# Performance work log

Hardware: AMD Instinct MI355X
Metric: run time of the kernel (lower is better)

## Reference

```python
import jax, jax.numpy as jnp
import numpy as np

CAPS = 16          # num_capsules
DIM = 16           # capsule_dim
NUM_ROUTING = 3
L2_EPS = 1e-12     # tf.nn.l2_normalize epsilon


def setup_inputs() -> dict:
    key = jax.random.key(0)
    k1, k2 = jax.random.split(key)
    inputs = jax.random.normal(k1, (16, 64, 64, 128), dtype=jnp.float32)
    # Conv2D kernel, HWIO layout, fan-in scaled like glorot-ish init
    kernel = jax.random.normal(k2, (3, 3, 128, CAPS * DIM), dtype=jnp.float32) * 0.03
    bias = jnp.zeros((CAPS * DIM,), dtype=jnp.float32)
    return {"inputs": inputs, "kernel": kernel, "bias": bias}


def reference(inputs, kernel, bias):
    # Conv2D(caps*dim, 3x3, padding='same', activation='relu'), channels_last
    x = jax.lax.conv_general_dilated(
        inputs, kernel, window_strides=(1, 1), padding="SAME",
        dimension_numbers=("NHWC", "HWIO", "NHWC"))
    x = jax.nn.relu(x + bias)
    B, H, W, _ = x.shape
    x = x.reshape(B, H * W, CAPS, DIM)            # (B, N, C, D)
    b = jnp.zeros((B, H * W, CAPS), dtype=x.dtype)
    v = None
    for _ in range(NUM_ROUTING):
        c = jax.nn.softmax(b, axis=-1)             # over capsules
        s = jnp.einsum("bnc,bncd->bcd", c, x)      # weighted sum over spatial
        # tf.nn.l2_normalize along last axis
        v = s * jax.lax.rsqrt(jnp.maximum(jnp.sum(s * s, axis=-1, keepdims=True), L2_EPS))
        b = b + jnp.einsum("bncd,bcd->bnc", x, v)  # agreement update
    # tile v over spatial dims: (B,1,1,C*D) -> (B,H,W,C*D)
    out = jnp.broadcast_to(v.reshape(B, 1, 1, CAPS * DIM), (B, H, W, CAPS * DIM))
    return out
```

## Files before the change

kernel.cpp:

```cpp
#include <hip/hip_runtime.h>
#include <hip/hip_bf16.h>

typedef unsigned short u16;
typedef unsigned int   u32;

typedef __bf16 bf16x8 __attribute__((ext_vector_type(8)));
typedef float  f32x4  __attribute__((ext_vector_type(4)));

#define GLDS(gp, lp) __builtin_amdgcn_global_load_lds( \
    (const __attribute__((address_space(1))) void*)(gp), \
    (__attribute__((address_space(3))) void*)(lp), 16, 0, 0)

__device__ __forceinline__ u16 f2b(float f) {
    __hip_bfloat16 h = __float2bfloat16(f);
    u16 u; __builtin_memcpy(&u, &h, 2); return u;
}
__device__ __forceinline__ float blo(u32 u) { return __uint_as_float(u << 16); }
__device__ __forceinline__ float bhi(u32 u) { return __uint_as_float(u & 0xffff0000u); }

__global__ void k_prep(const float* __restrict__ in, const float* __restrict__ wk,
                       u16* __restrict__ pad, u16* __restrict__ BF,
                       float* __restrict__ stats) {
    int bx = blockIdx.x, tid = threadIdx.x;
    if (bx < 4356) {
        int idx = bx * 256 + tid;
        int e0  = idx * 8;
        int ch  = e0 & 127;
        int rest = e0 >> 7;
        int pw = rest % 66;
        int r2 = rest / 66;
        int ph = r2 % 66;
        int b  = r2 / 66;
        u16 ov[8];
        if (ph >= 1 && ph <= 64 && pw >= 1 && pw <= 64) {
            const float* src = in + (((b * 64 + (ph - 1)) * 64 + (pw - 1)) * 128 + ch);
            const float4* s4 = (const float4*)src;
            float4 f0 = s4[0], f1 = s4[1];
            ov[0]=f2b(f0.x); ov[1]=f2b(f0.y); ov[2]=f2b(f0.z); ov[3]=f2b(f0.w);
            ov[4]=f2b(f1.x); ov[5]=f2b(f1.y); ov[6]=f2b(f1.z); ov[7]=f2b(f1.w);
        } else {
            #pragma unroll
            for (int j = 0; j < 8; ++j) ov[j] = 0;
        }
        uint4 w; __builtin_memcpy(&w, ov, 16);
        *(uint4*)(pad + e0) = w;
    } else if (bx < 5508) {
        int t = (bx - 4356) * 256 + tid;
        int j  = t & 7;
        int n  = (t >> 3) & 255;
        int q  = (t >> 11) & 3;
        int kk = (t >> 13) & 3;
        int p  = t >> 15;
        BF[t] = f2b(wk[(p * 128 + kk * 32 + q * 8 + j) * 256 + n]);
    } else {
        stats[(bx - 5508) * 256 + tid] = 0.f;
    }
}

__launch_bounds__(256, 2)
__global__ void k_conv(const u16* __restrict__ Ap, const u16* __restrict__ BF,
                       const float* __restrict__ bias,
                       u16* __restrict__ X, float* __restrict__ s0) {
    __shared__ u16 ldsA[12672];
    const int t = threadIdx.x;
    const int lane = t & 63, wid = t >> 6;
    const int q = lane >> 4, l15 = lane & 15;
    const int bb = blockIdx.x >> 6;
    const int h  = blockIdx.x & 63;
    const int wn0 = wid << 6;

#define STAGE(S) { \
    const int sb0 = wid * 396; \
    _Pragma("unroll") for (int i = 0; i < 6; ++i) { \
        int sb = sb0 + i * 64; \
        int slot = sb + lane; \
        int pr = slot / 528; int rem = slot - pr * 528; \
        int wp = rem >> 3, cs = rem & 7; \
        int gc = (S) * 8 + (cs ^ (wp & 7)); \
        const u16* g = Ap + ((((bb * 66 + h + pr) * 66 + wp) << 7) + (gc << 3)); \
        GLDS(g, (char*)ldsA + sb * 16); \
    } \
    { int sb = sb0 + 384; \
      if (lane < 12) { \
        int slot = sb + lane; \
        int pr = slot / 528; int rem = slot - pr * 528; \
        int wp = rem >> 3, cs = rem & 7; \
        int gc = (S) * 8 + (cs ^ (wp & 7)); \
        const u16* g = Ap + ((((bb * 66 + h + pr) * 66 + wp) << 7) + (gc << 3)); \
        GLDS(g, (char*)ldsA + sb * 16); \
      } } }

#define LOADB(B, P, S) { \
    _Pragma("unroll") for (int kk = 0; kk < 2; ++kk) \
    _Pragma("unroll") for (int ni = 0; ni < 4; ++ni) \
        B[kk * 4 + ni] = *(const bf16x8*)(BFl + (P) * 32768 + \
                                          ((S) * 2 + kk) * 8192 + ni * 128); }

#define COMPP(B, DH, DW) { \
    _Pragma("unroll") for (int kk = 0; kk < 2; ++kk) { \
        bf16x8 af[4]; \
        _Pragma("unroll") for (int mi = 0; mi < 4; ++mi) { \
            int wp = mi * 16 + l15 + (DW); \
            int swz = (kk * 4 + q) ^ (wp & 7); \
            af[mi] = *(const bf16x8*)((const char*)ldsA + \
                (((DH) * 528 + wp * 8 + swz) << 4)); \
        } \
        _Pragma("unroll") for (int mi = 0; mi < 4; ++mi) \
        _Pragma("unroll") for (int ni = 0; ni < 4; ++ni) \
            acc[mi][ni] = __builtin_amdgcn_mfma_f32_16x16x32_bf16( \
                af[mi], B[kk * 4 + ni], acc[mi][ni], 0, 0, 0); } }

    const u16* BFl = BF + (q * 2048 + (wn0 + l15) * 8);

    f32x4 zero = {0.f, 0.f, 0.f, 0.f};
    f32x4 acc[4][4];
    #pragma unroll
    for (int mi = 0; mi < 4; ++mi)
        #pragma unroll
        for (int ni = 0; ni < 4; ++ni) acc[mi][ni] = zero;

    bf16x8 B0[8], B1[8];

    STAGE(0);
    __syncthreads();
    LOADB(B0, 0, 0);
    LOADB(B1, 1, 0); COMPP(B0, 0, 0);
    LOADB(B0, 2, 0); COMPP(B1, 0, 1);
    LOADB(B1, 3, 0); COMPP(B0, 0, 2);
    LOADB(B0, 4, 0); COMPP(B1, 1, 0);
    LOADB(B1, 5, 0); COMPP(B0, 1, 1);
    LOADB(B0, 6, 0); COMPP(B1, 1, 2);
    LOADB(B1, 7, 0); COMPP(B0, 2, 0);
    LOADB(B0, 8, 0); COMPP(B1, 2, 1);
    COMPP(B0, 2, 2);
    __syncthreads();

    STAGE(1);
    __syncthreads();
    LOADB(B0, 0, 1);
    LOADB(B1, 1, 1); COMPP(B0, 0, 0);
    LOADB(B0, 2, 1); COMPP(B1, 0, 1);
    LOADB(B1, 3, 1); COMPP(B0, 0, 2);
    LOADB(B0, 4, 1); COMPP(B1, 1, 0);
    LOADB(B1, 5, 1); COMPP(B0, 1, 1);
    LOADB(B0, 6, 1); COMPP(B1, 1, 2);
    LOADB(B1, 7, 1); COMPP(B0, 2, 0);
    LOADB(B0, 8, 1); COMPP(B1, 2, 1);
    COMPP(B0, 2, 2);

    float bv[4];
    #pragma unroll
    for (int ni = 0; ni < 4; ++ni) bv[ni] = bias[wn0 + ni * 16 + l15];
    float colsum[4] = {0.f, 0.f, 0.f, 0.f};
    u16* xrow = X + (((bb << 12) + (h << 6) + q * 4) * 256) + wn0 + l15;
    #pragma unroll
    for (int mi = 0; mi < 4; ++mi) {
        #pragma unroll
        for (int rr = 0; rr < 4; ++rr) {
            u16* xp = xrow + (mi * 16 + rr) * 256;
            #pragma unroll
            for (int ni = 0; ni < 4; ++ni) {
                float v = acc[mi][ni][rr] + bv[ni];
                v = v > 0.f ? v : 0.f;
                xp[ni * 16] = f2b(v);
                colsum[ni] += v;
            }
        }
    }
    #pragma unroll
    for (int ni = 0; ni < 4; ++ni) {
        float c = colsum[ni];
        c += __shfl_xor(c, 16);
        c += __shfl_xor(c, 32);
        if (lane < 16) atomicAdd(&s0[bb * 256 + wn0 + ni * 16 + l15], c);
    }
#undef STAGE
#undef LOADB
#undef COMPP
}

__launch_bounds__(256, 4)
__global__ void k_pass(const u16* __restrict__ X, const float* __restrict__ Sa,
                       const float* __restrict__ Sb, float* __restrict__ Sout,
                       int use2) {
    __shared__ float v1s[272], v2s[272];
    __shared__ float red[4 * 272];
    const int t = threadIdx.x, b = blockIdx.y, chunk = blockIdx.x;
    const int c = t & 15, nl = t >> 4;
    const int lane = t & 63, wid = t >> 6;
    {
        float sa = Sa[b * 256 + t];
        float ss = sa * sa;
        #pragma unroll
        for (int off = 1; off < 16; off <<= 1) ss += __shfl_xor(ss, off);
        ss = ss < 1e-12f ? 1e-12f : ss;
        v1s[(t >> 4) * 17 + (t & 15)] = sa / sqrtf(ss);
        if (use2) {
            float sb = Sb[b * 256 + t];
            float s2v = sb * sb;
            #pragma unroll
            for (int off = 1; off < 16; off <<= 1) s2v += __shfl_xor(s2v, off);
            s2v = s2v < 1e-12f ? 1e-12f : s2v;
            v2s[(t >> 4) * 17 + (t & 15)] = sb / sqrtf(s2v);
        } else {
            v2s[(t >> 4) * 17 + (t & 15)] = 0.f;
        }
    }
    const u16* xbase = X + ((b << 12) + chunk * 64 + nl) * 256 + c * 16;
    uint4 pa[8];
    #pragma unroll
    for (int r = 0; r < 4; ++r) {
        pa[2 * r]     = ((const uint4*)(xbase + r * 16 * 256))[0];
        pa[2 * r + 1] = ((const uint4*)(xbase + r * 16 * 256))[1];
    }
    __syncthreads();
    float v1r[16], v2r[16];
    #pragma unroll
    for (int d = 0; d < 16; ++d) { v1r[d] = v1s[c * 17 + d]; v2r[d] = v2s[c * 17 + d]; }

    float acc[16];
    #pragma unroll
    for (int d = 0; d < 16; ++d) acc[d] = 0.f;

    #pragma unroll
    for (int r = 0; r < 4; ++r) {
        u32 us[8];
        __builtin_memcpy(us, &pa[2 * r], 32);
        float xf[16];
        #pragma unroll
        for (int j = 0; j < 8; ++j) { xf[2*j] = blo(us[j]); xf[2*j+1] = bhi(us[j]); }
        float d1 = 0.f, d2 = 0.f;
        #pragma unroll
        for (int d = 0; d < 16; ++d) {
            d1 += xf[d] * v1r[d];
            d2 += xf[d] * v2r[d];
        }
        float bvv = use2 ? (d1 + d2) : d1;
        float e = __expf(bvv);
        float sm = e;
        #pragma unroll
        for (int off = 1; off < 16; off <<= 1) sm += __shfl_xor(sm, off);
        float w = e / sm;
        #pragma unroll
        for (int d = 0; d < 16; ++d) acc[d] += w * xf[d];
    }
    #pragma unroll
    for (int d = 0; d < 16; ++d) {
        acc[d] += __shfl_xor(acc[d], 16);
        acc[d] += __shfl_xor(acc[d], 32);
    }
    if (lane < 16) {
        #pragma unroll
        for (int d = 0; d < 16; ++d) red[wid * 272 + lane * 17 + d] = acc[d];
    }
    __syncthreads();
    {
        int c2 = t >> 4, d2 = t & 15;
        float tot = red[c2 * 17 + d2]       + red[272 + c2 * 17 + d2]
                  + red[544 + c2 * 17 + d2] + red[816 + c2 * 17 + d2];
        atomicAdd(&Sout[b * 256 + t], tot);
    }
}

__launch_bounds__(256, 4)
__global__ void k_bcast(const float* __restrict__ S, float* __restrict__ Out) {
    __shared__ float vls[256];
    int t = threadIdx.x, bx = blockIdx.x, b = blockIdx.y;
    float s = S[b * 256 + t];
    float ss = s * s;
    #pragma unroll
    for (int off = 1; off < 16; off <<= 1) ss += __shfl_xor(ss, off);
    ss = ss < 1e-12f ? 1e-12f : ss;
    vls[t] = s / sqrtf(ss);
    __syncthreads();
    float4 myv = ((const float4*)vls)[t & 63];
    float4* o = (float4*)Out + (long)b * 262144 + bx * 4096;
    #pragma unroll
    for (int j = 0; j < 16; ++j) o[j * 256 + t] = myv;
}

extern "C" void kernel_launch(void* const* d_in, const int* in_sizes, int n_in,
                              void* d_out, int out_size, void* d_ws, size_t ws_size,
                              hipStream_t stream) {
    const float* in   = (const float*)d_in[0];
    const float* wk   = (const float*)d_in[1];
    const float* bias = (const float*)d_in[2];
    float* out = (float*)d_out;
    char* ws = (char*)d_ws;

    const size_t OFF_PAD = 0;
    const size_t OFF_BF  = 17842176;
    const size_t OFF_X   = 18432000;
    const size_t OFF_ST  = 51986432;
    const size_t NEEDED  = OFF_ST + 3 * 16384;
    if (ws_size < NEEDED) return;

    u16* pad = (u16*)(ws + OFF_PAD);
    u16* BF  = (u16*)(ws + OFF_BF);
    u16* X   = (u16*)(ws + OFF_X);
    float* s0 = (float*)(ws + OFF_ST);
    float* s2 = s0 + 4096;
    float* s3 = s2 + 4096;

    k_prep <<<5556, 256, 0, stream>>>(in, wk, pad, BF, s0);
    k_conv <<<1024, 256, 0, stream>>>(pad, BF, bias, X, s0);
    k_pass <<<dim3(64, 16), 256, 0, stream>>>(X, s0, s0, s2, 0);
    k_pass <<<dim3(64, 16), 256, 0, stream>>>(X, s0, s2, s3, 1);
    k_bcast<<<dim3(64, 16), 256, 0, stream>>>(s3, out);
}
```

Baseline: 162.7 us.

## Triple-buffer B fragments across conv stages and fold routing vectors into one sum

The conv GEMM now keeps three register buffers of B fragments instead of two. It issues the first three loads before the barrier and prefetches stage 1's first fragments during stage 0's tail, so B loads overlap MFMA work across the stage boundary. The routing pass uses linearity of the dot product: it adds v1 and v2 once into a single vector, which halves the per-element dot-product FMAs and the shared/register footprint. The extra B buffer raises register pressure, which could hurt occupancy under the 4-wave launch bound.

Result: no change. 162.9 us (+0.1%).

```diff
diff --git a/kernel.cpp b/kernel.cpp
--- a/kernel.cpp
+++ b/kernel.cpp
@@ -119,34 +119,35 @@
         #pragma unroll
         for (int ni = 0; ni < 4; ++ni) acc[mi][ni] = zero;
 
-    bf16x8 B0[8], B1[8];
+    bf16x8 B0[8], B1[8], B2[8];
 
     STAGE(0);
-    __syncthreads();
     LOADB(B0, 0, 0);
-    LOADB(B1, 1, 0); COMPP(B0, 0, 0);
-    LOADB(B0, 2, 0); COMPP(B1, 0, 1);
-    LOADB(B1, 3, 0); COMPP(B0, 0, 2);
-    LOADB(B0, 4, 0); COMPP(B1, 1, 0);
-    LOADB(B1, 5, 0); COMPP(B0, 1, 1);
-    LOADB(B0, 6, 0); COMPP(B1, 1, 2);
-    LOADB(B1, 7, 0); COMPP(B0, 2, 0);
-    LOADB(B0, 8, 0); COMPP(B1, 2, 1);
-    COMPP(B0, 2, 2);
+    LOADB(B1, 1, 0);
+    LOADB(B2, 2, 0);
+    __syncthreads();
+    COMPP(B0, 0, 0); LOADB(B0, 3, 0);
+    COMPP(B1, 0, 1); LOADB(B1, 4, 0);
+    COMPP(B2, 0, 2); LOADB(B2, 5, 0);
+    COMPP(B0, 1, 0); LOADB(B0, 6, 0);
+    COMPP(B1, 1, 1); LOADB(B1, 7, 0);
+    COMPP(B2, 1, 2); LOADB(B2, 8, 0);
+    COMPP(B0, 2, 0); LOADB(B0, 0, 1);
+    COMPP(B1, 2, 1); LOADB(B1, 1, 1);
+    COMPP(B2, 2, 2); LOADB(B2, 2, 1);
     __syncthreads();
 
     STAGE(1);
     __syncthreads();
-    LOADB(B0, 0, 1);
-    LOADB(B1, 1, 1); COMPP(B0, 0, 0);
-    LOADB(B0, 2, 1); COMPP(B1, 0, 1);
-    LOADB(B1, 3, 1); COMPP(B0, 0, 2);
-    LOADB(B0, 4, 1); COMPP(B1, 1, 0);
-    LOADB(B1, 5, 1); COMPP(B0, 1, 1);
-    LOADB(B0, 6, 1); COMPP(B1, 1, 2);
-    LOADB(B1, 7, 1); COMPP(B0, 2, 0);
-    LOADB(B0, 8, 1); COMPP(B1, 2, 1);
-    COMPP(B0, 2, 2);
+    COMPP(B0, 0, 0); LOADB(B0, 3, 1);
+    COMPP(B1, 0, 1); LOADB(B1, 4, 1);
+    COMPP(B2, 0, 2); LOADB(B2, 5, 1);
+    COMPP(B0, 1, 0); LOADB(B0, 6, 1);
+    COMPP(B1, 1, 1); LOADB(B1, 7, 1);
+    COMPP(B2, 1, 2); LOADB(B2, 8, 1);
+    COMPP(B0, 2, 0);
+    COMPP(B1, 2, 1);
+    COMPP(B2, 2, 2);
 
     float bv[4];
     #pragma unroll
@@ -183,7 +184,7 @@
 __global__ void k_pass(const u16* __restrict__ X, const float* __restrict__ Sa,
                        const float* __restrict__ Sb, float* __restrict__ Sout,
                        int use2) {
-    __shared__ float v1s[272], v2s[272];
+    __shared__ float vs[272];
     __shared__ float red[4 * 272];
     const int t = threadIdx.x, b = blockIdx.y, chunk = blockIdx.x;
     const int c = t & 15, nl = t >> 4;
@@ -194,29 +195,28 @@
         #pragma unroll
         for (int off = 1; off < 16; off <<= 1) ss += __shfl_xor(ss, off);
         ss = ss < 1e-12f ? 1e-12f : ss;
-        v1s[(t >> 4) * 17 + (t & 15)] = sa / sqrtf(ss);
+        float vv = sa / sqrtf(ss);
         if (use2) {
             float sb = Sb[b * 256 + t];
             float s2v = sb * sb;
             #pragma unroll
             for (int off = 1; off < 16; off <<= 1) s2v += __shfl_xor(s2v, off);
             s2v = s2v < 1e-12f ? 1e-12f : s2v;
-            v2s[(t >> 4) * 17 + (t & 15)] = sb / sqrtf(s2v);
-        } else {
-            v2s[(t >> 4) * 17 + (t & 15)] = 0.f;
+            vv += sb / sqrtf(s2v);
         }
+        vs[(t >> 4) * 17 + (t & 15)] = vv;
     }
     const u16* xbase = X + ((b << 12) + chunk * 64 + nl) * 256 + c * 16;
     uint4 pa[8];
     #pragma unroll
     for (int r = 0; r < 4; ++r) {
-        pa[2 * r]     = ((const uint4*)(xbase + r * 16 * 256))[0];
-        pa[2 * r + 1] = ((const uint4*)(xbase + r * 16 * 256))[1];
-    }
-    __syncthreads();
-    float v1r[16], v2r[16];
-    #pragma unroll
-    for (int d = 0; d < 16; ++d) { v1r[d] = v1s[c * 17 + d]; v2r[d] = v2s[c * 17 + d]; }
+        pa[2 * r]     = ((const uint4*)(xbase + r * 4096))[0];
+        pa[2 * r + 1] = ((const uint4*)(xbase + r * 4096))[1];
+    }
+    __syncthreads();
+    float vr[16];
+    #pragma unroll
+    for (int d = 0; d < 16; ++d) vr[d] = vs[c * 17 + d];
 
     float acc[16];
     #pragma unroll
@@ -229,13 +229,9 @@
         float xf[16];
         #pragma unroll
         for (int j = 0; j < 8; ++j) { xf[2*j] = blo(us[j]); xf[2*j+1] = bhi(us[j]); }
-        float d1 = 0.f, d2 = 0.f;
-        #pragma unroll
-        for (int d = 0; d < 16; ++d) {
-            d1 += xf[d] * v1r[d];
-            d2 += xf[d] * v2r[d];
-        }
-        float bvv = use2 ? (d1 + d2) : d1;
+        float bvv = 0.f;
+        #pragma unroll
+        for (int d = 0; d < 16; ++d) bvv += xf[d] * vr[d];
         float e = __expf(bvv);
         float sm = e;
         #pragma unroll
```
